# Kernel optimization log

Measured on AMD Instinct MI355X. Metric: run time of the kernel, lower is better.

The kernel has to match this reference:

```python
import jax, jax.numpy as jnp
import numpy as np

NUM_ANCHORS = 896
NUM_COORDS = 16
SCALE = 128.0           # x/y/w/h scale (all 128.0 in the module)
SCORE_CLIP = 100.0
MIN_SCORE = 0.75
MIN_SUPP = 0.3
MAX_DET = 256           # fixed cap on NMS iterations (>= max valid detections)
BATCH = 512


def setup_inputs() -> dict:
    key = jax.random.key(0)
    k1, k2, k3 = jax.random.split(key, 3)
    # realistic extents and the weighted-NMS blending branch is exercised
    raw_box = jax.random.normal(k1, (BATCH, NUM_ANCHORS, NUM_COORDS), jnp.float32) * 20.0
    raw_score = jax.random.normal(k2, (BATCH, NUM_ANCHORS, 1), jnp.float32)
    anchors = jax.random.uniform(k3, (NUM_ANCHORS, 4), dtype=jnp.float32)
    return {"raw_box_tensor": raw_box, "raw_score_tensor": raw_score, "anchors": anchors}


def _decode_boxes(raw, anchors):
    # raw: (B, A, 16), anchors: (A, 4) as [x_center, y_center, w, h]
    ax, ay, aw, ah = anchors[:, 0], anchors[:, 1], anchors[:, 2], anchors[:, 3]
    xc = raw[..., 0] / SCALE * aw + ax
    yc = raw[..., 1] / SCALE * ah + ay
    w = raw[..., 2] / SCALE * aw
    h = raw[..., 3] / SCALE * ah
    box = jnp.stack([yc - h * 0.5, xc - w * 0.5, yc + h * 0.5, xc + w * 0.5], axis=-1)
    # 6 keypoints, (x, y) pairs
    kp = raw[..., 4:].reshape(raw.shape[:-1] + (6, 2))
    kpx = kp[..., 0] / SCALE * aw[:, None] + ax[:, None]
    kpy = kp[..., 1] / SCALE * ah[:, None] + ay[:, None]
    kps = jnp.stack([kpx, kpy], axis=-1).reshape(raw.shape[:-1] + (12,))
    return jnp.concatenate([box, kps], axis=-1)  # (B, A, 16)


def _iou(box, boxes):
    # faithful to overlap_similarity: intersect is NOT clamped, only final ratio is
    i0 = jnp.maximum(box[0], boxes[:, 0])
    i1 = jnp.maximum(box[1], boxes[:, 1])
    i2 = jnp.minimum(box[2], boxes[:, 2])
    i3 = jnp.minimum(box[3], boxes[:, 3])
    inter = (i2 - i0) * (i3 - i1)
    area_a = (box[2] - box[0]) * (box[3] - box[1])
    area_b = (boxes[:, 2] - boxes[:, 0]) * (boxes[:, 3] - boxes[:, 1])
    union = area_a + area_b - inter
    return jnp.maximum(0.0, inter / union)


def _nms_one(det, valid):
    # det: (A, 17) = [16 coords, score]; valid: (A,) bool (score >= MIN_SCORE)
    scores = det[:, 16]

    def step(remaining, _):
        any_left = remaining.any()
        # pick highest-score remaining detection (== head of score-sorted order)
        idx = jnp.argmax(jnp.where(remaining, scores, -jnp.inf))
        ious = _iou(det[idx, :4], det[:, :4])
        overlap = remaining & (ious > MIN_SUPP)
        n = overlap.sum()
        w = jnp.where(overlap, scores, 0.0)
        total = w.sum()
        safe_total = jnp.where(total > 0, total, 1.0)
        wcoords = (det[:, :16] * w[:, None]).sum(0) / safe_total   # (16,)
        wscore = total / jnp.maximum(n, 1)
        wdet = jnp.where(n > 1,
                         jnp.concatenate([wcoords, wscore[None]]),
                         det[idx])
        out = jnp.where(any_left, wdet, jnp.zeros((17,), det.dtype))
        return remaining & ~overlap, (out, any_left)

    _, (outs, flags) = jax.lax.scan(step, valid, None, length=MAX_DET)
    return outs, flags  # (MAX_DET, 17), (MAX_DET,) bool


def reference(raw_box_tensor, raw_score_tensor, anchors):
    boxes = _decode_boxes(raw_box_tensor, anchors)                       # (B, A, 16)
    clipped = jnp.clip(raw_score_tensor, -SCORE_CLIP, SCORE_CLIP)
    scores = jax.nn.sigmoid(clipped)[..., 0]                             # (B, A)
    det = jnp.concatenate([boxes, scores[..., None]], axis=-1)           # (B, A, 17)
    valid = scores >= MIN_SCORE
    out, flags = jax.vmap(_nms_one)(det, valid)                          # (B, MAX_DET, 17), (B, MAX_DET)
    return out, flags
```

## Files before the change

kernel.cpp:

```cpp
#include <hip/hip_runtime.h>
#include <math.h>

#pragma clang fp contract(off)

#define NA      896
#define MAXDET  256
#define NBATCH  512
#define CAP     192
#define NCHUNK  14

typedef unsigned long long u64;
typedef unsigned int u32;

__device__ __forceinline__ u64 rl64(u64 v, int l) {
    u32 lo = __builtin_amdgcn_readlane((u32)v, l);
    u32 hi = __builtin_amdgcn_readlane((u32)(v >> 32), l);
    return ((u64)hi << 32) | (u64)lo;
}

struct FastSh {
    float  det[CAP][17];
    float4 sbox[CAP];
    u64    keys[CAP];
    int    slot_a[CAP];
    float  slot_s[CAP];
    u32    mat32[CAP][6];
    u32    cl[CAP][6];
};
struct SlowSh {
    float  score[NA];
    float4 box[NA];
    u64    remw[NCHUNK];
};
union ShU { FastSh f; SlowSh s; };

__global__ __launch_bounds__(512, 4) void nms_kernel(
    const float* __restrict__ raw_box,
    const float* __restrict__ raw_score,
    const float* __restrict__ anchors,
    float* __restrict__ out,
    float* __restrict__ flags,
    float* __restrict__ gws, int has_ws)
{
    __shared__ ShU sh;
    __shared__ u64 Psh[3];
    __shared__ int stuck_sh;
    __shared__ int Ccnt;

    const int b    = blockIdx.x;
    const int tid  = threadIdx.x;
    const int lane = tid & 63;
    const int wv   = tid >> 6;

    const float* sc_base = raw_score + (size_t)b * NA;
    float* out_b = out   + (size_t)b * MAXDET * 17;
    float* flg_b = flags + (size_t)b * MAXDET;

    if (tid == 0) Ccnt = 0;
    __syncthreads();

    #pragma unroll
    for (int r = 0; r < 2; ++r) {
        int c = wv + r * 8;
        if (c < NCHUNK) {
            int a = c * 64 + lane;
            float x = sc_base[a];
            x = fminf(fmaxf(x, -100.0f), 100.0f);
            float s = 1.0f / (1.0f + expf(-x));
            bool v = (s >= 0.75f);
            u64 bal = __ballot(v);
            int np = (int)__popcll(bal);
            int base = 0;
            if (lane == 0 && np) base = atomicAdd(&Ccnt, np);
            base = __shfl(base, 0);
            if (v) {
                int slot = base + (int)__popcll(bal & ((1ull << lane) - 1ull));
                if (slot < CAP) {
                    sh.f.keys[slot]   = ((u64)__float_as_uint(s) << 10) | (u64)(1023 - a);
                    sh.f.slot_a[slot] = a;
                    sh.f.slot_s[slot] = s;
                }
            }
        }
    }
    __syncthreads();
    const int C = Ccnt;

    if (C > CAP) {
        if (!has_ws) {
            for (int t = tid; t < MAXDET * 17; t += 512) out_b[t] = 0.0f;
            for (int t = tid; t < MAXDET;      t += 512) flg_b[t] = 0.0f;
            return;
        }
        float* gdet = gws + (size_t)b * NA * 17;
        for (int a0 = tid; a0 < NA; a0 += 512) {
            float x = sc_base[a0];
            x = fminf(fmaxf(x, -100.0f), 100.0f);
            float s = 1.0f / (1.0f + expf(-x));
            const float4 an = ((const float4*)anchors)[a0];
            const float4* rb = (const float4*)(raw_box + ((size_t)b * NA + a0) * 16);
            float4 r0 = rb[0], r1 = rb[1], r2 = rb[2], r3 = rb[3];
            float ax = an.x, ay = an.y, aw = an.z, ah = an.w;
            float xc = r0.x / 128.0f * aw + ax;
            float yc = r0.y / 128.0f * ah + ay;
            float w  = r0.z / 128.0f * aw;
            float h  = r0.w / 128.0f * ah;
            float d0 = yc - h * 0.5f, d1 = xc - w * 0.5f;
            float d2 = yc + h * 0.5f, d3 = xc + w * 0.5f;
            sh.s.score[a0] = s;
            sh.s.box[a0]   = make_float4(d0, d1, d2, d3);
            float* gr = gdet + (size_t)a0 * 17;
            gr[0] = d0; gr[1] = d1; gr[2] = d2; gr[3] = d3;
            float kp[12] = {r1.x, r1.y, r1.z, r1.w,
                            r2.x, r2.y, r2.z, r2.w,
                            r3.x, r3.y, r3.z, r3.w};
            #pragma unroll
            for (int t = 0; t < 6; ++t) {
                gr[4 + 2 * t] = kp[2 * t]     / 128.0f * aw + ax;
                gr[5 + 2 * t] = kp[2 * t + 1] / 128.0f * ah + ay;
            }
            gr[16] = s;
            u64 bal = __ballot(s >= 0.75f);
            if (lane == 0) sh.s.remw[a0 >> 6] = bal;
        }
        __syncthreads();
        if (wv == 0) {
            int step = 0;
            for (; step < MAXDET; ++step) {
                u64 best = 0;
                for (int c = 0; c < NCHUNK; ++c) {
                    if ((sh.s.remw[c] >> lane) & 1ull) {
                        int a = c * 64 + lane;
                        u64 key = ((u64)__float_as_uint(sh.s.score[a]) << 10)
                                | (u64)(1023 - a);
                        if (key > best) best = key;
                    }
                }
                #pragma unroll
                for (int off = 32; off; off >>= 1) {
                    u64 o = __shfl_xor(best, off);
                    if (o > best) best = o;
                }
                if (best == 0) break;
                int idx = 1023 - (int)(best & 1023ull);
                float4 bb = sh.s.box[idx];
                float areaA = (bb.z - bb.x) * (bb.w - bb.y);
                u32 ov = 0; int n = 0;
                for (int c = 0; c < NCHUNK; ++c) {
                    bool o = false;
                    if ((sh.s.remw[c] >> lane) & 1ull) {
                        int a = c * 64 + lane;
                        float4 cb = sh.s.box[a];
                        float i0 = fmaxf(bb.x, cb.x), i1 = fmaxf(bb.y, cb.y);
                        float i2 = fminf(bb.z, cb.z), i3 = fminf(bb.w, cb.w);
                        float inter = (i2 - i0) * (i3 - i1);
                        float areaB = (cb.z - cb.x) * (cb.w - cb.y);
                        float q = inter / (areaA + areaB - inter);
                        o = (q > 0.3f);
                    }
                    u64 balc = __ballot(o);
                    if (o) ov |= 1u << c;
                    n += (int)__popcll(balc);
                    if (lane == 0) sh.s.remw[c] &= ~balc;
                }
                if (n <= 1) {
                    if (lane < 17) out_b[step * 17 + lane] = gdet[(size_t)idx * 17 + lane];
                    if (lane == 17) flg_b[step] = 1.0f;
                } else {
                    float tot = 0.0f, wcv[16];
                    #pragma unroll
                    for (int j = 0; j < 16; ++j) wcv[j] = 0.0f;
                    for (int c = 0; c < NCHUNK; ++c) {
                        if ((ov >> c) & 1u) {
                            int a = c * 64 + lane;
                            float s2 = sh.s.score[a]; tot += s2;
                            #pragma unroll
                            for (int j = 0; j < 16; ++j)
                                wcv[j] += gdet[(size_t)a * 17 + j] * s2;
                        }
                    }
                    #pragma unroll
                    for (int off = 32; off; off >>= 1) {
                        tot += __shfl_xor(tot, off);
                        #pragma unroll
                        for (int j = 0; j < 16; ++j) wcv[j] += __shfl_xor(wcv[j], off);
                    }
                    if (lane == 0) {
                        float safe = (tot > 0.0f) ? tot : 1.0f;
                        #pragma unroll
                        for (int j = 0; j < 16; ++j) out_b[step * 17 + j] = wcv[j] / safe;
                        out_b[step * 17 + 16] = tot / (float)n;
                        flg_b[step] = 1.0f;
                    }
                }
            }
            for (int t = step * 17 + lane; t < MAXDET * 17; t += 64) out_b[t] = 0.0f;
            for (int t = step + lane;      t < MAXDET;      t += 64) flg_b[t] = 0.0f;
        }
        return;
    }

    if (tid < C) {
        int a = sh.f.slot_a[tid];
        float s = sh.f.slot_s[tid];
        const float4 an = ((const float4*)anchors)[a];
        const float4* rb = (const float4*)(raw_box + ((size_t)b * NA + a) * 16);
        float4 r0 = rb[0], r1 = rb[1], r2 = rb[2], r3 = rb[3];
        u64 myk = sh.f.keys[tid];
        int q = 0;
        #pragma unroll 8
        for (int i = 0; i < C; ++i) q += (sh.f.keys[i] > myk) ? 1 : 0;
        float ax = an.x, ay = an.y, aw = an.z, ah = an.w;
        float xc = r0.x / 128.0f * aw + ax;
        float yc = r0.y / 128.0f * ah + ay;
        float w  = r0.z / 128.0f * aw;
        float h  = r0.w / 128.0f * ah;
        float d0 = yc - h * 0.5f, d1 = xc - w * 0.5f;
        float d2 = yc + h * 0.5f, d3 = xc + w * 0.5f;
        sh.f.det[q][0] = d0; sh.f.det[q][1] = d1;
        sh.f.det[q][2] = d2; sh.f.det[q][3] = d3;
        sh.f.det[q][16] = s;
        sh.f.sbox[q] = make_float4(d0, d1, d2, d3);
        float kp[12] = {r1.x, r1.y, r1.z, r1.w,
                        r2.x, r2.y, r2.z, r2.w,
                        r3.x, r3.y, r3.z, r3.w};
        #pragma unroll
        for (int t = 0; t < 6; ++t) {
            sh.f.det[q][4 + 2 * t] = kp[2 * t]     / 128.0f * aw + ax;
            sh.f.det[q][5 + 2 * t] = kp[2 * t + 1] / 128.0f * ah + ay;
        }
    }
    __syncthreads();

    const int words = (C + 31) >> 5;
    for (int u = tid; u < C * words; u += 512) {
        int w = u / C;
        int row = u - w * C;
        int kbase = w << 5;
        int ke = C - kbase; if (ke > 32) ke = 32;
        float4 sb = sh.f.sbox[row];
        float ar = (sb.z - sb.x) * (sb.w - sb.y);
        u32 mm = 0, bit = 1u;
        #pragma unroll 4
        for (int k = 0; k < ke; ++k, bit <<= 1) {
            float4 bk = sh.f.sbox[kbase + k];
            float ak = (bk.z - bk.x) * (bk.w - bk.y);
            float i0 = fmaxf(sb.x, bk.x), i1 = fmaxf(sb.y, bk.y);
            float i2 = fminf(sb.z, bk.z), i3 = fminf(sb.w, bk.w);
            float inter = (i2 - i0) * (i3 - i1);
            float qq = inter / (ar + ak - inter);
            if (qq > 0.3f) mm |= bit;
        }
        sh.f.mat32[row][w] = mm;
    }
    __syncthreads();

    if (wv == 0) {
        const u32 (*M)[6] = sh.f.mat32;
        u64 m00 = (u64)M[lane][0]      | ((u64)M[lane][1] << 32);
        u64 m01 = (u64)M[lane][2]      | ((u64)M[lane][3] << 32);
        u64 m10 = (u64)M[lane + 64][0] | ((u64)M[lane + 64][1] << 32);
        u64 m11 = (u64)M[lane + 64][2] | ((u64)M[lane + 64][3] << 32);
        u64 rem0 = (C >= 64)  ? ~0ull : ((C > 0)   ? ((1ull << C) - 1)         : 0ull);
        u64 rem1 = (C >= 128) ? ~0ull : ((C > 64)  ? ((1ull << (C - 64)) - 1)  : 0ull);
        u64 rem2 = (C >= 192) ? ~0ull : ((C > 128) ? ((1ull << (C - 128)) - 1) : 0ull);
        u64 P0 = 0, P1 = 0, P2 = 0;
        int stk = CAP;

        if (C <= 128) {
            while (rem0) {
                int i = (int)__builtin_ctzll(rem0);
                u64 r0 = rl64(m00, i), r1 = rl64(m01, i);
                if (!((r0 >> i) & 1ull)) { stk = i; break; }
                P0 |= 1ull << i;
                rem0 &= ~r0; rem1 &= ~r1;
            }
            if (stk == CAP) while (rem1) {
                int i = (int)__builtin_ctzll(rem1);
                u64 r1 = rl64(m11, i);
                if (!((r1 >> i) & 1ull)) { stk = 64 + i; break; }
                P1 |= 1ull << i;
                rem1 &= ~r1;
            }
        } else {
            u64 m02 = (u64)M[lane][4]       | ((u64)M[lane][5] << 32);
            u64 m12 = (u64)M[lane + 64][4]  | ((u64)M[lane + 64][5] << 32);
            u64 m20 = (u64)M[lane + 128][0] | ((u64)M[lane + 128][1] << 32);
            u64 m21 = (u64)M[lane + 128][2] | ((u64)M[lane + 128][3] << 32);
            u64 m22 = (u64)M[lane + 128][4] | ((u64)M[lane + 128][5] << 32);
            while (rem0) {
                int i = (int)__builtin_ctzll(rem0);
                u64 r0 = rl64(m00, i), r1 = rl64(m01, i), r2 = rl64(m02, i);
                if (!((r0 >> i) & 1ull)) { stk = i; break; }
                P0 |= 1ull << i;
                rem0 &= ~r0; rem1 &= ~r1; rem2 &= ~r2;
            }
            if (stk == CAP) while (rem1) {
                int i = (int)__builtin_ctzll(rem1);
                u64 r1 = rl64(m11, i), r2 = rl64(m12, i);
                if (!((r1 >> i) & 1ull)) { stk = 64 + i; break; }
                P1 |= 1ull << i;
                rem1 &= ~r1; rem2 &= ~r2;
            }
            if (stk == CAP) while (rem2) {
                int i = (int)__builtin_ctzll(rem2);
                u64 r2 = rl64(m22, i);
                if (!((r2 >> i) & 1ull)) { stk = 128 + i; break; }
                P2 |= 1ull << i;
                rem2 &= ~r2;
            }
            (void)m20; (void)m21;
        }
        if (lane == 0) { Psh[0] = P0; Psh[1] = P1; Psh[2] = P2; stuck_sh = stk; }
    } else {
        for (int t = tid - 64; t < CAP * 6;     t += 448) ((u32*)sh.f.cl)[t] = 0u;
        for (int t = tid - 64; t < MAXDET * 17; t += 448) out_b[t] = 0.0f;
        for (int t = tid - 64; t < MAXDET;      t += 448) flg_b[t] = 0.0f;
    }
    __syncthreads();

    const u64 P0 = Psh[0], P1 = Psh[1], P2 = Psh[2];
    const int stuck_v = stuck_sh;

    if (tid < C) {
        u64 q0 = ((u64)sh.f.mat32[tid][0] | ((u64)sh.f.mat32[tid][1] << 32)) & P0;
        u64 q1 = ((u64)sh.f.mat32[tid][2] | ((u64)sh.f.mat32[tid][3] << 32)) & P1;
        u64 q2 = ((u64)sh.f.mat32[tid][4] | ((u64)sh.f.mat32[tid][5] << 32)) & P2;
        int fc = -1;
        if      (q0) fc = (int)__builtin_ctzll(q0);
        else if (q1) fc = 64  + (int)__builtin_ctzll(q1);
        else if (q2) fc = 128 + (int)__builtin_ctzll(q2);
        if (fc >= 0) atomicOr(&sh.f.cl[fc][tid >> 5], 1u << (tid & 31));
    }
    __syncthreads();

    const int Pn = (int)__popcll(P0) + (int)__popcll(P1) + (int)__popcll(P2);
    bool is_pick = false;
    if (tid < C) {
        is_pick = (tid < 64)  ? ((P0 >> tid) & 1ull)
                : (tid < 128) ? ((P1 >> (tid - 64)) & 1ull)
                              : ((P2 >> (tid - 128)) & 1ull);
    }
    if (is_pick) {
        int s;
        if (tid < 64)
            s = (int)__popcll(P0 & ((tid ? ((1ull << tid) - 1) : 0ull)));
        else if (tid < 128)
            s = (int)__popcll(P0)
              + (int)__popcll(P1 & (((tid - 64) ? ((1ull << (tid - 64)) - 1) : 0ull)));
        else
            s = (int)__popcll(P0) + (int)__popcll(P1)
              + (int)__popcll(P2 & (((tid - 128) ? ((1ull << (tid - 128)) - 1) : 0ull)));

        u64 c0 = (u64)sh.f.cl[tid][0] | ((u64)sh.f.cl[tid][1] << 32);
        u64 c1 = (u64)sh.f.cl[tid][2] | ((u64)sh.f.cl[tid][3] << 32);
        u64 c2 = (u64)sh.f.cl[tid][4] | ((u64)sh.f.cl[tid][5] << 32);
        int n = (int)__popcll(c0) + (int)__popcll(c1) + (int)__popcll(c2);
        float* orow = out_b + s * 17;
        if (n <= 1) {
            #pragma unroll
            for (int c = 0; c < 17; ++c) orow[c] = sh.f.det[tid][c];
        } else {
            float tot = 0.0f, wc[16];
            #pragma unroll
            for (int c = 0; c < 16; ++c) wc[c] = 0.0f;
            u64 m = c0;
            while (m) { int k = (int)__builtin_ctzll(m); m &= m - 1;
                float sc = sh.f.det[k][16]; tot += sc;
                #pragma unroll
                for (int c = 0; c < 16; ++c) wc[c] += sh.f.det[k][c] * sc; }
            m = c1;
            while (m) { int k = 64 + (int)__builtin_ctzll(m); m &= m - 1;
                float sc = sh.f.det[k][16]; tot += sc;
                #pragma unroll
                for (int c = 0; c < 16; ++c) wc[c] += sh.f.det[k][c] * sc; }
            m = c2;
            while (m) { int k = 128 + (int)__builtin_ctzll(m); m &= m - 1;
                float sc = sh.f.det[k][16]; tot += sc;
                #pragma unroll
                for (int c = 0; c < 16; ++c) wc[c] += sh.f.det[k][c] * sc; }
            float safe = (tot > 0.0f) ? tot : 1.0f;
            #pragma unroll
            for (int c = 0; c < 16; ++c) orow[c] = wc[c] / safe;
            orow[16] = tot / (float)n;
        }
        flg_b[s] = 1.0f;
    }
    if (stuck_v < CAP) {
        for (int s2 = Pn + tid; s2 < MAXDET; s2 += 512) {
            float* orow = out_b + s2 * 17;
            #pragma unroll
            for (int c = 0; c < 17; ++c) orow[c] = sh.f.det[stuck_v][c];
            flg_b[s2] = 1.0f;
        }
    }
}

extern "C" void kernel_launch(void* const* d_in, const int* in_sizes, int n_in,
                              void* d_out, int out_size, void* d_ws, size_t ws_size,
                              hipStream_t stream) {
    const float* raw_box   = (const float*)d_in[0];
    const float* raw_score = (const float*)d_in[1];
    const float* anchors   = (const float*)d_in[2];
    float* out   = (float*)d_out;
    float* flags = out + (size_t)NBATCH * MAXDET * 17;
    int has_ws = (ws_size >= (size_t)NBATCH * NA * 17 * sizeof(float)) ? 1 : 0;
    nms_kernel<<<NBATCH, 512, 0, stream>>>(raw_box, raw_score, anchors, out, flags,
                                           (float*)d_ws, has_ws);
}
```

Measured before the change: 32.05 us.

## Parallelize NMS pick selection with fixed-point ballot iteration and wave-level ranking

Replaces the serial greedy readlane loop that picks kept boxes with a parallel fixed-point iteration: each lane decides whether its box is kept given the current pick set, using ballots, until the set stops changing. The serial path stays as a fallback for degenerate or non-converging cases. It also replaces the atomic compaction with per-chunk counts and a prefix sum, and computes sort ranks with wave ballots instead of a per-thread O(C) scan. The aim is to shorten the serial critical path inside each block, at the cost of more sync points and a bounded number of rounds that may not converge.

```diff
diff --git a/kernel.cpp b/kernel.cpp
--- a/kernel.cpp
+++ b/kernel.cpp
@@ -24,6 +24,7 @@
     u64    keys[CAP];
     int    slot_a[CAP];
     float  slot_s[CAP];
+    int    rankv[CAP];
     u32    mat32[CAP][6];
     u32    cl[CAP][6];
 };
@@ -45,7 +46,7 @@
     __shared__ ShU sh;
     __shared__ u64 Psh[3];
     __shared__ int stuck_sh;
-    __shared__ int Ccnt;
+    __shared__ int cnt[NCHUNK];
 
     const int b    = blockIdx.x;
     const int tid  = threadIdx.x;
@@ -56,12 +57,11 @@
     float* out_b = out   + (size_t)b * MAXDET * 17;
     float* flg_b = flags + (size_t)b * MAXDET;
 
-    if (tid == 0) Ccnt = 0;
-    __syncthreads();
-
+    float s_r[2]; u64 bal_r[2]; bool v_r[2];
     #pragma unroll
     for (int r = 0; r < 2; ++r) {
         int c = wv + r * 8;
+        s_r[r] = 0.0f; bal_r[r] = 0ull; v_r[r] = false;
         if (c < NCHUNK) {
             int a = c * 64 + lane;
             float x = sc_base[a];
@@ -69,22 +69,18 @@
             float s = 1.0f / (1.0f + expf(-x));
             bool v = (s >= 0.75f);
             u64 bal = __ballot(v);
-            int np = (int)__popcll(bal);
-            int base = 0;
-            if (lane == 0 && np) base = atomicAdd(&Ccnt, np);
-            base = __shfl(base, 0);
-            if (v) {
-                int slot = base + (int)__popcll(bal & ((1ull << lane) - 1ull));
-                if (slot < CAP) {
-                    sh.f.keys[slot]   = ((u64)__float_as_uint(s) << 10) | (u64)(1023 - a);
-                    sh.f.slot_a[slot] = a;
-                    sh.f.slot_s[slot] = s;
-                }
-            }
-        }
-    }
-    __syncthreads();
-    const int C = Ccnt;
+            s_r[r] = s; bal_r[r] = bal; v_r[r] = v;
+            if (lane == 0) cnt[c] = (int)__popcll(bal);
+        }
+    }
+    __syncthreads();
+
+    int cn[NCHUNK];
+    #pragma unroll
+    for (int j = 0; j < NCHUNK; ++j) cn[j] = cnt[j];
+    int C = 0;
+    #pragma unroll
+    for (int j = 0; j < NCHUNK; ++j) C += cn[j];
 
     if (C > CAP) {
         if (!has_ws) {
@@ -200,30 +196,62 @@
         return;
     }
 
+    #pragma unroll
+    for (int r = 0; r < 2; ++r) {
+        int c = wv + r * 8;
+        if (c < NCHUNK && v_r[r]) {
+            int base = 0;
+            #pragma unroll
+            for (int j = 0; j < NCHUNK; ++j) base += (j < c) ? cn[j] : 0;
+            int slot = base + (int)__popcll(bal_r[r] & ((1ull << lane) - 1ull));
+            int a = c * 64 + lane;
+            sh.f.keys[slot]   = ((u64)__float_as_uint(s_r[r]) << 10) | (u64)(1023 - a);
+            sh.f.slot_a[slot] = a;
+            sh.f.slot_s[slot] = s_r[r];
+        }
+    }
+    __syncthreads();
+
+    float4 an, g0, g1, g2, g3; float s_my = 0.0f;
     if (tid < C) {
-        int a = sh.f.slot_a[tid];
-        float s = sh.f.slot_s[tid];
-        const float4 an = ((const float4*)anchors)[a];
-        const float4* rb = (const float4*)(raw_box + ((size_t)b * NA + a) * 16);
-        float4 r0 = rb[0], r1 = rb[1], r2 = rb[2], r3 = rb[3];
-        u64 myk = sh.f.keys[tid];
-        int q = 0;
-        #pragma unroll 8
-        for (int i = 0; i < C; ++i) q += (sh.f.keys[i] > myk) ? 1 : 0;
+        int a_my = sh.f.slot_a[tid];
+        s_my = sh.f.slot_s[tid];
+        an = ((const float4*)anchors)[a_my];
+        const float4* rb = (const float4*)(raw_box + ((size_t)b * NA + a_my) * 16);
+        g0 = rb[0]; g1 = rb[1]; g2 = rb[2]; g3 = rb[3];
+    }
+    {
+        u64 k0 = (lane < C)       ? sh.f.keys[lane]       : 0ull;
+        u64 k1 = (lane + 64 < C)  ? sh.f.keys[lane + 64]  : 0ull;
+        u64 k2 = (lane + 128 < C) ? sh.f.keys[lane + 128] : 0ull;
+        for (int r = 0; ; ++r) {
+            int i = wv + r * 8;
+            if (i >= C) break;
+            u64 ki = sh.f.keys[i];
+            int q = (int)__popcll(__ballot(k0 > ki))
+                  + (int)__popcll(__ballot(k1 > ki))
+                  + (int)__popcll(__ballot(k2 > ki));
+            if (lane == 0) sh.f.rankv[i] = q;
+        }
+    }
+    __syncthreads();
+
+    if (tid < C) {
+        int q = sh.f.rankv[tid];
         float ax = an.x, ay = an.y, aw = an.z, ah = an.w;
-        float xc = r0.x / 128.0f * aw + ax;
-        float yc = r0.y / 128.0f * ah + ay;
-        float w  = r0.z / 128.0f * aw;
-        float h  = r0.w / 128.0f * ah;
+        float xc = g0.x / 128.0f * aw + ax;
+        float yc = g0.y / 128.0f * ah + ay;
+        float w  = g0.z / 128.0f * aw;
+        float h  = g0.w / 128.0f * ah;
         float d0 = yc - h * 0.5f, d1 = xc - w * 0.5f;
         float d2 = yc + h * 0.5f, d3 = xc + w * 0.5f;
         sh.f.det[q][0] = d0; sh.f.det[q][1] = d1;
         sh.f.det[q][2] = d2; sh.f.det[q][3] = d3;
-        sh.f.det[q][16] = s;
+        sh.f.det[q][16] = s_my;
         sh.f.sbox[q] = make_float4(d0, d1, d2, d3);
-        float kp[12] = {r1.x, r1.y, r1.z, r1.w,
-                        r2.x, r2.y, r2.z, r2.w,
-                        r3.x, r3.y, r3.z, r3.w};
+        float kp[12] = {g1.x, g1.y, g1.z, g1.w,
+                        g2.x, g2.y, g2.z, g2.w,
+                        g3.x, g3.y, g3.z, g3.w};
         #pragma unroll
         for (int t = 0; t < 6; ++t) {
             sh.f.det[q][4 + 2 * t] = kp[2 * t]     / 128.0f * aw + ax;
@@ -257,59 +285,65 @@
 
     if (wv == 0) {
         const u32 (*M)[6] = sh.f.mat32;
-        u64 m00 = (u64)M[lane][0]      | ((u64)M[lane][1] << 32);
-        u64 m01 = (u64)M[lane][2]      | ((u64)M[lane][3] << 32);
-        u64 m10 = (u64)M[lane + 64][0] | ((u64)M[lane + 64][1] << 32);
-        u64 m11 = (u64)M[lane + 64][2] | ((u64)M[lane + 64][3] << 32);
-        u64 rem0 = (C >= 64)  ? ~0ull : ((C > 0)   ? ((1ull << C) - 1)         : 0ull);
-        u64 rem1 = (C >= 128) ? ~0ull : ((C > 64)  ? ((1ull << (C - 64)) - 1)  : 0ull);
-        u64 rem2 = (C >= 192) ? ~0ull : ((C > 128) ? ((1ull << (C - 128)) - 1) : 0ull);
-        u64 P0 = 0, P1 = 0, P2 = 0;
+        const bool vA = (lane < C), vB = (lane + 64 < C), vC = (lane + 128 < C);
+        u64 A0 = vA ? ((u64)M[lane][0]       | ((u64)M[lane][1] << 32))       : 0ull;
+        u64 B0 = vB ? ((u64)M[lane + 64][0]  | ((u64)M[lane + 64][1] << 32))  : 0ull;
+        u64 B1 = vB ? ((u64)M[lane + 64][2]  | ((u64)M[lane + 64][3] << 32))  : 0ull;
+        u64 C0 = vC ? ((u64)M[lane + 128][0] | ((u64)M[lane + 128][1] << 32)) : 0ull;
+        u64 C1 = vC ? ((u64)M[lane + 128][2] | ((u64)M[lane + 128][3] << 32)) : 0ull;
+        u64 C2 = vC ? ((u64)M[lane + 128][4] | ((u64)M[lane + 128][5] << 32)) : 0ull;
+
+        const u64 bel = lane ? ((1ull << lane) - 1ull) : 0ull;
+        const u64 F0 = (C >= 64)  ? ~0ull : ((C > 0)   ? ((1ull << C) - 1)         : 0ull);
+        const u64 F1 = (C >= 128) ? ~0ull : ((C > 64)  ? ((1ull << (C - 64)) - 1)  : 0ull);
+        const u64 F2 = (C >= 192) ? ~0ull : ((C > 128) ? ((1ull << (C - 128)) - 1) : 0ull);
+
+        bool degen = (__ballot((vA && !((A0 >> lane) & 1ull)) ||
+                               (vB && !((B1 >> lane) & 1ull)) ||
+                               (vC && !((C2 >> lane) & 1ull))) != 0ull);
+        u64 P0 = F0, P1 = F1, P2 = F2;
+        bool ok = false;
+        if (!degen) {
+            for (int round = 0; round < 32; ++round) {
+                bool a0 = vA && !(A0 & P0 & bel);
+                bool a1 = vB && !((B0 & P0) | (B1 & P1 & bel));
+                bool a2 = vC && !((C0 & P0) | (C1 & P1) | (C2 & P2 & bel));
+                u64 n0 = __ballot(a0), n1 = __ballot(a1), n2 = __ballot(a2);
+                if (n0 == P0 && n1 == P1 && n2 == P2) { ok = true; break; }
+                P0 = n0; P1 = n1; P2 = n2;
+            }
+        }
         int stk = CAP;
-
-        if (C <= 128) {
+        if (!ok) {
+            u64 r00 = vA ? ((u64)M[lane][0]       | ((u64)M[lane][1] << 32))       : 0ull;
+            u64 r01 = vA ? ((u64)M[lane][2]       | ((u64)M[lane][3] << 32))       : 0ull;
+            u64 r02 = vA ? ((u64)M[lane][4]       | ((u64)M[lane][5] << 32))       : 0ull;
+            u64 r11 = B1;
+            u64 r12 = vB ? ((u64)M[lane + 64][4]  | ((u64)M[lane + 64][5] << 32))  : 0ull;
+            u64 r22 = C2;
+            u64 rem0 = F0, rem1 = F1, rem2 = F2;
+            P0 = 0; P1 = 0; P2 = 0;
             while (rem0) {
                 int i = (int)__builtin_ctzll(rem0);
-                u64 r0 = rl64(m00, i), r1 = rl64(m01, i);
-                if (!((r0 >> i) & 1ull)) { stk = i; break; }
+                u64 w0 = rl64(r00, i), w1 = rl64(r01, i), w2 = rl64(r02, i);
+                if (!((w0 >> i) & 1ull)) { stk = i; break; }
                 P0 |= 1ull << i;
-                rem0 &= ~r0; rem1 &= ~r1;
+                rem0 &= ~w0; rem1 &= ~w1; rem2 &= ~w2;
             }
             if (stk == CAP) while (rem1) {
                 int i = (int)__builtin_ctzll(rem1);
-                u64 r1 = rl64(m11, i);
-                if (!((r1 >> i) & 1ull)) { stk = 64 + i; break; }
+                u64 w1 = rl64(r11, i), w2 = rl64(r12, i);
+                if (!((w1 >> i) & 1ull)) { stk = 64 + i; break; }
                 P1 |= 1ull << i;
-                rem1 &= ~r1;
-            }
-        } else {
-            u64 m02 = (u64)M[lane][4]       | ((u64)M[lane][5] << 32);
-            u64 m12 = (u64)M[lane + 64][4]  | ((u64)M[lane + 64][5] << 32);
-            u64 m20 = (u64)M[lane + 128][0] | ((u64)M[lane + 128][1] << 32);
-            u64 m21 = (u64)M[lane + 128][2] | ((u64)M[lane + 128][3] << 32);
-            u64 m22 = (u64)M[lane + 128][4] | ((u64)M[lane + 128][5] << 32);
-            while (rem0) {
-                int i = (int)__builtin_ctzll(rem0);
-                u64 r0 = rl64(m00, i), r1 = rl64(m01, i), r2 = rl64(m02, i);
-                if (!((r0 >> i) & 1ull)) { stk = i; break; }
-                P0 |= 1ull << i;
-                rem0 &= ~r0; rem1 &= ~r1; rem2 &= ~r2;
-            }
-            if (stk == CAP) while (rem1) {
-                int i = (int)__builtin_ctzll(rem1);
-                u64 r1 = rl64(m11, i), r2 = rl64(m12, i);
-                if (!((r1 >> i) & 1ull)) { stk = 64 + i; break; }
-                P1 |= 1ull << i;
-                rem1 &= ~r1; rem2 &= ~r2;
+                rem1 &= ~w1; rem2 &= ~w2;
             }
             if (stk == CAP) while (rem2) {
                 int i = (int)__builtin_ctzll(rem2);
-                u64 r2 = rl64(m22, i);
-                if (!((r2 >> i) & 1ull)) { stk = 128 + i; break; }
+                u64 w2 = rl64(r22, i);
+                if (!((w2 >> i) & 1ull)) { stk = 128 + i; break; }
                 P2 |= 1ull << i;
-                rem2 &= ~r2;
-            }
-            (void)m20; (void)m21;
+                rem2 &= ~w2;
+            }
         }
         if (lane == 0) { Psh[0] = P0; Psh[1] = P1; Psh[2] = P2; stuck_sh = stk; }
     } else {
@@ -334,14 +368,13 @@
     }
     __syncthreads();
 
-    const int Pn = (int)__popcll(P0) + (int)__popcll(P1) + (int)__popcll(P2);
     bool is_pick = false;
     if (tid < C) {
         is_pick = (tid < 64)  ? ((P0 >> tid) & 1ull)
                 : (tid < 128) ? ((P1 >> (tid - 64)) & 1ull)
                               : ((P2 >> (tid - 128)) & 1ull);
     }
-    if (is_pick) {
+    if (is_pick && tid < ((stuck_v < CAP) ? stuck_v : CAP)) {
         int s;
         if (tid < 64)
             s = (int)__popcll(P0 & ((tid ? ((1ull << tid) - 1) : 0ull)));
@@ -387,7 +420,15 @@
         flg_b[s] = 1.0f;
     }
     if (stuck_v < CAP) {
-        for (int s2 = Pn + tid; s2 < MAXDET; s2 += 512) {
+        int Pb = 0;
+        {
+            u64 t0 = P0, t1 = P1, t2 = P2;
+            if (stuck_v < 64)       { t0 &= (stuck_v ? ((1ull << stuck_v) - 1) : 0ull); t1 = 0; t2 = 0; }
+            else if (stuck_v < 128) { t1 &= (((stuck_v - 64) ? ((1ull << (stuck_v - 64)) - 1) : 0ull)); t2 = 0; }
+            else                    { t2 &= (((stuck_v - 128) ? ((1ull << (stuck_v - 128)) - 1) : 0ull)); }
+            Pb = (int)__popcll(t0) + (int)__popcll(t1) + (int)__popcll(t2);
+        }
+        for (int s2 = Pb + tid; s2 < MAXDET; s2 += 512) {
             float* orow = out_b + s2 * 17;
             #pragma unroll
             for (int c = 0; c < 17; ++c) orow[c] = sh.f.det[stuck_v][c];
```

Result: faster. 25.92 us (-19.1%).
